# Performance work log

Measured on AMD Instinct MI355X. Metric: run time of the kernel, lower is better.

The kernel has to match this reference:

```python
import jax, jax.numpy as jnp
import numpy as np


def setup_inputs() -> dict:
    key = jax.random.key(0)
    k1, k2, k3, k4 = jax.random.split(key, 4)
    B, H, S, E, L = 2, 12, 256, 64, 25
    return {
        "attention_probs": jax.random.uniform(k1, (B, H, S, S), dtype=jnp.float32),
        "value_attentions": jax.random.normal(k2, (B, H, S, E), dtype=jnp.float32),
        "relative_positions": jax.random.normal(k3, (B, S, S, H * E), dtype=jnp.float32),
        "W": jax.random.normal(k4, (L, H * E), dtype=jnp.float32) * 0.02,
        "b": jnp.zeros((L,), dtype=jnp.float32),
    }


def reference(attention_probs, value_attentions, relative_positions, W, b):
    # Faithful translation of TransformerMHSLayer.forward:
    #   out[b,h,i,j,e] = p[b,h,i,j] * (v[b,h,j,e] + rel[b,i,j,h,e])
    #   pre[b,j,i,l]   = sum_{h,e} out[b,h,i,j,e] * W[l, h*E+e] + bias[l]
    #   logits[b,j,l,i] = pre[b,j,i,l]
    B, H, S, E = value_attentions.shape
    L = W.shape[0]
    Wr = W.reshape(L, H, E)                       # [L,H,E], matches h*E+e flattening
    rel = relative_positions.reshape(B, S, S, H, E)  # view(B,S,S,H,E)
    # value term: contract v with W per head, then weight by attention probs
    pre = jnp.einsum('bhij,bhje,lhe->bjil', attention_probs, value_attentions, Wr)
    # relative-position term (same attention weighting)
    pre = pre + jnp.einsum('bhij,bijhe,lhe->bjil', attention_probs, rel, Wr)
    pre = pre + b                                  # bias over label dim
    return pre.transpose(0, 1, 3, 2)               # [B, S(j), L, S(i)]
```

## Files before the change

### kernel.cpp

```cpp
#include <hip/hip_runtime.h>
#include <stdint.h>


#define Bb 2
#define Hh 12
#define Ss 256
#define Ee 64
#define Ll 25
#define Kk 768

typedef __attribute__((ext_vector_type(8))) short bf16x8;
typedef __attribute__((ext_vector_type(4))) float f32x4;

#define NFRAG (Hh * 4)
#define AB_BYTES ((size_t)NFRAG * 64 * 8 * 2)
#define PT_BYTES ((size_t)Bb * Ss * Hh * Ss * 4)
#define WV_BYTES ((size_t)Bb * Ss * Hh * 32 * 4)

__device__ __forceinline__ ushort f2bf(float x) {
    union { float f; uint32_t u; } u; u.f = x;
    uint32_t r = u.u + 0x7fff + ((u.u >> 16) & 1);
    return (ushort)(r >> 16);
}

__global__ void a_pack_kernel(const float* __restrict__ W, ushort* __restrict__ ab) {
    int idx = blockIdx.x * 256 + threadIdx.x;
    if (idx >= NFRAG * 64) return;
    int lane = idx & 63, fi = idx >> 6;
    int Lt = fi & 1, ks = (fi >> 1) & 1, h = fi >> 2;
    int l = Lt * 16 + (lane & 15);
    int k0 = h * Ee + ks * 32 + (lane >> 4) * 8;
    ushort* dst = ab + (size_t)idx * 8;
#pragma unroll
    for (int t = 0; t < 8; ++t)
        dst[t] = (l < Ll) ? f2bf(W[l * Kk + k0 + t]) : (ushort)0;
}

__global__ void p_transpose_kernel(const float* __restrict__ p,
                                   float* __restrict__ pt) {
    __shared__ float tile[32][33];
    const int bh = blockIdx.y;
    const int b = bh / Hh, h = bh % Hh;
    const int ti = blockIdx.x >> 3, tj = blockIdx.x & 7;
    const int tx = threadIdx.x & 31, ty = threadIdx.x >> 5;
#pragma unroll
    for (int s = 0; s < 4; ++s) {
        const int il = ty + 8 * s;
        tile[il][tx] = p[((size_t)(b * Hh + h) * Ss + ti * 32 + il) * Ss + tj * 32 + tx];
    }
    __syncthreads();
#pragma unroll
    for (int s = 0; s < 4; ++s) {
        const int jl = ty + 8 * s;
        pt[((size_t)(b * Ss + tj * 32 + jl) * Hh + h) * Ss + ti * 32 + tx] = tile[tx][jl];
    }
}

__global__ void wv_kernel(const float* __restrict__ W, const float* __restrict__ v,
                          float* __restrict__ wv) {
    const int bj = blockIdx.x;
    const int b = bj >> 8, j = bj & (Ss - 1);
    const int t = threadIdx.x;
    const int h = t >> 5, l = t & 31;
    float acc = 0.f;
    if (l < Ll) {
        const float* wrow = W + l * Kk + h * Ee;
        const float* vrow = v + ((size_t)(b * Hh + h) * Ss + j) * Ee;
#pragma unroll
        for (int e = 0; e < Ee; ++e) acc = __builtin_fmaf(wrow[e], vrow[e], acc);
    }
    wv[((size_t)bj * Hh + h) * 32 + l] = acc;
}

struct Buf {
    float4 r0, r1, r2, r3;
    bf16x8 A00, A01, A10, A11;
    float pv;
};

__global__ __launch_bounds__(256, 4) void mhs_pipe2(
    const float* __restrict__ pt,
    const float* __restrict__ rel,
    const ushort* __restrict__ ab,
    const float* __restrict__ wv,
    const float* __restrict__ bias,
    float* __restrict__ out)
{
    const int m = (blockIdx.x & 7) * 256 + (blockIdx.x >> 3);
    const int ig = m & 3, j = (m >> 2) & (Ss - 1), b = m >> 10;
    const int tid = threadIdx.x;
    const int w = tid >> 6, lane = tid & 63;
    const int col = lane & 15, grp = lane >> 4;
    const int iw = ig * 64 + w * 16 + col;

    const float* relp = rel + ((size_t)(b * Ss + iw) * Ss + j) * Kk + grp * 8;
    const ushort* abl = ab + lane * 8;
    const float* ptb = pt + ((size_t)(b * Ss + j) * Hh) * Ss + iw;
    const float* wvb = wv + ((size_t)(b * Ss + j) * Hh) * 32 + grp * 4;

    f32x4 acc0 = {0.f, 0.f, 0.f, 0.f};
    f32x4 acc1 = {0.f, 0.f, 0.f, 0.f};

    auto load = [&](Buf& o, int h) {
        const float* rb = relp + h * Ee;
        o.r0 = *(const float4*)(rb);
        o.r1 = *(const float4*)(rb + 4);
        o.r2 = *(const float4*)(rb + 32);
        o.r3 = *(const float4*)(rb + 36);
        const ushort* ap = abl + (size_t)h * 2048;
        o.A00 = *(const bf16x8*)(ap);
        o.A01 = *(const bf16x8*)(ap + 512);
        o.A10 = *(const bf16x8*)(ap + 1024);
        o.A11 = *(const bf16x8*)(ap + 1536);
        o.pv = ptb[h * Ss];
    };

    auto compute = [&](const Buf& o) {
        const float s = o.pv;
        bf16x8 B0, B1;
#pragma unroll
        for (int t = 0; t < 4; ++t) {
            B0[t]     = (short)f2bf(s * ((const float*)&o.r0)[t]);
            B0[t + 4] = (short)f2bf(s * ((const float*)&o.r1)[t]);
            B1[t]     = (short)f2bf(s * ((const float*)&o.r2)[t]);
            B1[t + 4] = (short)f2bf(s * ((const float*)&o.r3)[t]);
        }
        acc0 = __builtin_amdgcn_mfma_f32_16x16x32_bf16(o.A00, B0, acc0, 0, 0, 0);
        acc0 = __builtin_amdgcn_mfma_f32_16x16x32_bf16(o.A10, B1, acc0, 0, 0, 0);
        acc1 = __builtin_amdgcn_mfma_f32_16x16x32_bf16(o.A01, B0, acc1, 0, 0, 0);
        acc1 = __builtin_amdgcn_mfma_f32_16x16x32_bf16(o.A11, B1, acc1, 0, 0, 0);
    };

    Buf oa, ob;
    load(oa, 0);
#pragma unroll 1
    for (int h = 0; h < Hh; h += 2) {
        load(ob, h + 1);
        compute(oa);
        if (h + 2 < Hh) load(oa, h + 2);
        compute(ob);
    }

    f32x4 val0 = {0.f, 0.f, 0.f, 0.f};
    f32x4 val1 = {0.f, 0.f, 0.f, 0.f};
#pragma unroll
    for (int h = 0; h < Hh; ++h) {
        const float pvh = ptb[h * Ss];
        const f32x4 w0 = *(const f32x4*)(wvb + h * 32);
        const f32x4 w1 = *(const f32x4*)(wvb + h * 32 + 16);
        val0 += pvh * w0;
        val1 += pvh * w1;
    }
    acc0 += val0;
    acc1 += val1;

#pragma unroll
    for (int r = 0; r < 4; ++r) {
        const int l0 = grp * 4 + r;
        out[((size_t)(b * Ss + j) * Ll + l0) * Ss + iw] = acc0[r] + bias[l0];
        const int l1 = 16 + grp * 4 + r;
        if (l1 < Ll)
            out[((size_t)(b * Ss + j) * Ll + l1) * Ss + iw] = acc1[r] + bias[l1];
    }
}

__global__ __launch_bounds__(256, 4) void mhs_basic(
    const float* __restrict__ p, const float* __restrict__ v,
    const float* __restrict__ rel, const float* __restrict__ W,
    const float* __restrict__ bias, float* __restrict__ out)
{
    const int g = blockIdx.x;
    const int ig = g & 3, j = (g >> 2) & (Ss - 1), b = g >> 10;
    const int tid = threadIdx.x;
    const int w = tid >> 6, lane = tid & 63;
    const int col = lane & 15, grp = lane >> 4;
    const int iw = ig * 64 + w * 16 + col;
    const float* relp = rel + ((size_t)(b * Ss + iw) * Ss + j) * Kk + grp * 8;

    f32x4 acc0 = {0.f, 0.f, 0.f, 0.f}, acc1 = {0.f, 0.f, 0.f, 0.f};
#pragma unroll 1
    for (int h = 0; h < Hh; ++h) {
        bf16x8 A00, A01, A10, A11;
#pragma unroll
        for (int t = 0; t < 8; ++t) {
            const int kb = h * Ee + grp * 8 + t;
            const int la = col, lb = 16 + col;
            A00[t] = (short)f2bf(W[la * Kk + kb]);
            A01[t] = (lb < Ll) ? (short)f2bf(W[lb * Kk + kb]) : (short)0;
            A10[t] = (short)f2bf(W[la * Kk + kb + 32]);
            A11[t] = (lb < Ll) ? (short)f2bf(W[lb * Kk + kb + 32]) : (short)0;
        }
        const float* vbp = v + ((size_t)(b * Hh + h) * Ss + j) * Ee + grp * 8;
        const float4 va0 = *(const float4*)(vbp);
        const float4 va1 = *(const float4*)(vbp + 4);
        const float4 vc0 = *(const float4*)(vbp + 32);
        const float4 vc1 = *(const float4*)(vbp + 36);
        const float* rb = relp + h * Ee;
        const float4 c0 = *(const float4*)(rb);
        const float4 c1 = *(const float4*)(rb + 4);
        const float4 c2 = *(const float4*)(rb + 32);
        const float4 c3 = *(const float4*)(rb + 36);
        const float pv = p[((size_t)(b * Hh + h) * Ss + iw) * Ss + j];
        bf16x8 B0, B1;
#pragma unroll
        for (int t = 0; t < 4; ++t) {
            B0[t]     = (short)f2bf(((const float*)&c0)[t] + ((const float*)&va0)[t]);
            B0[t + 4] = (short)f2bf(((const float*)&c1)[t] + ((const float*)&va1)[t]);
            B1[t]     = (short)f2bf(((const float*)&c2)[t] + ((const float*)&vc0)[t]);
            B1[t + 4] = (short)f2bf(((const float*)&c3)[t] + ((const float*)&vc1)[t]);
        }
        f32x4 C0 = {0.f, 0.f, 0.f, 0.f}, C1 = {0.f, 0.f, 0.f, 0.f};
        C0 = __builtin_amdgcn_mfma_f32_16x16x32_bf16(A00, B0, C0, 0, 0, 0);
        C0 = __builtin_amdgcn_mfma_f32_16x16x32_bf16(A10, B1, C0, 0, 0, 0);
        C1 = __builtin_amdgcn_mfma_f32_16x16x32_bf16(A01, B0, C1, 0, 0, 0);
        C1 = __builtin_amdgcn_mfma_f32_16x16x32_bf16(A11, B1, C1, 0, 0, 0);
        acc0 += pv * C0;
        acc1 += pv * C1;
    }
#pragma unroll
    for (int r = 0; r < 4; ++r) {
        const int l0 = grp * 4 + r;
        out[((size_t)(b * Ss + j) * Ll + l0) * Ss + iw] = acc0[r] + bias[l0];
        const int l1 = 16 + grp * 4 + r;
        if (l1 < Ll)
            out[((size_t)(b * Ss + j) * Ll + l1) * Ss + iw] = acc1[r] + bias[l1];
    }
}

extern "C" void kernel_launch(void* const* d_in, const int* in_sizes, int n_in,
                              void* d_out, int out_size, void* d_ws, size_t ws_size,
                              hipStream_t stream) {
    const float* p    = (const float*)d_in[0];
    const float* v    = (const float*)d_in[1];
    const float* rel  = (const float*)d_in[2];
    const float* W    = (const float*)d_in[3];
    const float* bias = (const float*)d_in[4];
    float* out = (float*)d_out;

    const int nblk = Bb * Ss * 4;
    const bool full = ws_size >= AB_BYTES + PT_BYTES + WV_BYTES;

    if (full) {
        ushort* ab = (ushort*)d_ws;
        float* pt = (float*)((char*)d_ws + AB_BYTES);
        float* wvp = (float*)((char*)d_ws + AB_BYTES + PT_BYTES);
        hipLaunchKernelGGL(a_pack_kernel, dim3((NFRAG * 64 + 255) / 256), dim3(256),
                           0, stream, W, ab);
        hipLaunchKernelGGL(p_transpose_kernel, dim3(64, Bb * Hh), dim3(256),
                           0, stream, p, pt);
        hipLaunchKernelGGL(wv_kernel, dim3(Bb * Ss), dim3(Hh * 32),
                           0, stream, W, v, wvp);
        hipLaunchKernelGGL(mhs_pipe2, dim3(nblk), dim3(256), 0, stream,
                           pt, rel, ab, wvp, bias, out);
    } else {
        hipLaunchKernelGGL(mhs_basic, dim3(nblk), dim3(256), 0, stream,
                           p, v, rel, W, bias, out);
    }
}
```

Measured before the change: 123.6 us.

## Remap blocks to fixed query row i with j across lanes; drop p transpose

```diff
diff --git a/kernel.cpp b/kernel.cpp
--- a/kernel.cpp
+++ b/kernel.cpp
@@ -14,7 +14,6 @@
 
 #define NFRAG (Hh * 4)
 #define AB_BYTES ((size_t)NFRAG * 64 * 8 * 2)
-#define PT_BYTES ((size_t)Bb * Ss * Hh * Ss * 4)
 #define WV_BYTES ((size_t)Bb * Ss * Hh * 32 * 4)
 
 __device__ __forceinline__ ushort f2bf(float x) {
@@ -34,26 +33,6 @@
 #pragma unroll
     for (int t = 0; t < 8; ++t)
         dst[t] = (l < Ll) ? f2bf(W[l * Kk + k0 + t]) : (ushort)0;
-}
-
-__global__ void p_transpose_kernel(const float* __restrict__ p,
-                                   float* __restrict__ pt) {
-    __shared__ float tile[32][33];
-    const int bh = blockIdx.y;
-    const int b = bh / Hh, h = bh % Hh;
-    const int ti = blockIdx.x >> 3, tj = blockIdx.x & 7;
-    const int tx = threadIdx.x & 31, ty = threadIdx.x >> 5;
-#pragma unroll
-    for (int s = 0; s < 4; ++s) {
-        const int il = ty + 8 * s;
-        tile[il][tx] = p[((size_t)(b * Hh + h) * Ss + ti * 32 + il) * Ss + tj * 32 + tx];
-    }
-    __syncthreads();
-#pragma unroll
-    for (int s = 0; s < 4; ++s) {
-        const int jl = ty + 8 * s;
-        pt[((size_t)(b * Ss + tj * 32 + jl) * Hh + h) * Ss + ti * 32 + tx] = tile[tx][jl];
-    }
 }
 
 __global__ void wv_kernel(const float* __restrict__ W, const float* __restrict__ v,
@@ -78,24 +57,29 @@
     float pv;
 };
 
-__global__ __launch_bounds__(256, 4) void mhs_pipe2(
-    const float* __restrict__ pt,
+__global__ __launch_bounds__(256, 4) void mhs_jcol(
+    const float* __restrict__ p,
     const float* __restrict__ rel,
     const ushort* __restrict__ ab,
     const float* __restrict__ wv,
     const float* __restrict__ bias,
     float* __restrict__ out)
 {
-    const int m = (blockIdx.x & 7) * 256 + (blockIdx.x >> 3);
-    const int ig = m & 3, j = (m >> 2) & (Ss - 1), b = m >> 10;
+    const int bid = blockIdx.x;
+    const int xcd = bid & 7, idx = bid >> 3;
+    const int slot = idx >> 5, within = idx & 31;
+    const int g = slot * 8 + xcd;
+    const int n = g * 32 + within;
+    const int jb = n & 3, i = (n >> 2) & (Ss - 1), b = n >> 10;
+
     const int tid = threadIdx.x;
     const int w = tid >> 6, lane = tid & 63;
     const int col = lane & 15, grp = lane >> 4;
-    const int iw = ig * 64 + w * 16 + col;
-
-    const float* relp = rel + ((size_t)(b * Ss + iw) * Ss + j) * Kk + grp * 8;
+    const int j = jb * 64 + w * 16 + col;
+
+    const float* relp = rel + ((size_t)(b * Ss + i) * Ss + j) * Kk + grp * 8;
     const ushort* abl = ab + lane * 8;
-    const float* ptb = pt + ((size_t)(b * Ss + j) * Hh) * Ss + iw;
+    const float* pb = p + ((size_t)(b * Hh) * Ss + i) * Ss + j;
     const float* wvb = wv + ((size_t)(b * Ss + j) * Hh) * 32 + grp * 4;
 
     f32x4 acc0 = {0.f, 0.f, 0.f, 0.f};
@@ -112,7 +96,7 @@
         o.A01 = *(const bf16x8*)(ap + 512);
         o.A10 = *(const bf16x8*)(ap + 1024);
         o.A11 = *(const bf16x8*)(ap + 1536);
-        o.pv = ptb[h * Ss];
+        o.pv = pb[(size_t)h * Ss * Ss];
     };
 
     auto compute = [&](const Buf& o) {
@@ -145,7 +129,7 @@
     f32x4 val1 = {0.f, 0.f, 0.f, 0.f};
 #pragma unroll
     for (int h = 0; h < Hh; ++h) {
-        const float pvh = ptb[h * Ss];
+        const float pvh = pb[(size_t)h * Ss * Ss];
         const f32x4 w0 = *(const f32x4*)(wvb + h * 32);
         const f32x4 w1 = *(const f32x4*)(wvb + h * 32 + 16);
         val0 += pvh * w0;
@@ -157,25 +141,25 @@
 #pragma unroll
     for (int r = 0; r < 4; ++r) {
         const int l0 = grp * 4 + r;
-        out[((size_t)(b * Ss + j) * Ll + l0) * Ss + iw] = acc0[r] + bias[l0];
+        out[((size_t)(b * Ss + j) * Ll + l0) * Ss + i] = acc0[r] + bias[l0];
         const int l1 = 16 + grp * 4 + r;
         if (l1 < Ll)
-            out[((size_t)(b * Ss + j) * Ll + l1) * Ss + iw] = acc1[r] + bias[l1];
-    }
-}
-
-__global__ __launch_bounds__(256, 4) void mhs_basic(
+            out[((size_t)(b * Ss + j) * Ll + l1) * Ss + i] = acc1[r] + bias[l1];
+    }
+}
+
+__global__ __launch_bounds__(256, 4) void mhs_basic_j(
     const float* __restrict__ p, const float* __restrict__ v,
     const float* __restrict__ rel, const float* __restrict__ W,
     const float* __restrict__ bias, float* __restrict__ out)
 {
-    const int g = blockIdx.x;
-    const int ig = g & 3, j = (g >> 2) & (Ss - 1), b = g >> 10;
+    const int n = blockIdx.x;
+    const int jb = n & 3, i = (n >> 2) & (Ss - 1), b = n >> 10;
     const int tid = threadIdx.x;
     const int w = tid >> 6, lane = tid & 63;
     const int col = lane & 15, grp = lane >> 4;
-    const int iw = ig * 64 + w * 16 + col;
-    const float* relp = rel + ((size_t)(b * Ss + iw) * Ss + j) * Kk + grp * 8;
+    const int j = jb * 64 + w * 16 + col;
+    const float* relp = rel + ((size_t)(b * Ss + i) * Ss + j) * Kk + grp * 8;
 
     f32x4 acc0 = {0.f, 0.f, 0.f, 0.f}, acc1 = {0.f, 0.f, 0.f, 0.f};
 #pragma unroll 1
@@ -200,30 +184,27 @@
         const float4 c1 = *(const float4*)(rb + 4);
         const float4 c2 = *(const float4*)(rb + 32);
         const float4 c3 = *(const float4*)(rb + 36);
-        const float pv = p[((size_t)(b * Hh + h) * Ss + iw) * Ss + j];
+        const float pv = p[((size_t)(b * Hh + h) * Ss + i) * Ss + j];
         bf16x8 B0, B1;
 #pragma unroll
         for (int t = 0; t < 4; ++t) {
-            B0[t]     = (short)f2bf(((const float*)&c0)[t] + ((const float*)&va0)[t]);
-            B0[t + 4] = (short)f2bf(((const float*)&c1)[t] + ((const float*)&va1)[t]);
-            B1[t]     = (short)f2bf(((const float*)&c2)[t] + ((const float*)&vc0)[t]);
-            B1[t + 4] = (short)f2bf(((const float*)&c3)[t] + ((const float*)&vc1)[t]);
+            B0[t]     = (short)f2bf(pv * (((const float*)&c0)[t] + ((const float*)&va0)[t]));
+            B0[t + 4] = (short)f2bf(pv * (((const float*)&c1)[t] + ((const float*)&va1)[t]));
+            B1[t]     = (short)f2bf(pv * (((const float*)&c2)[t] + ((const float*)&vc0)[t]));
+            B1[t + 4] = (short)f2bf(pv * (((const float*)&c3)[t] + ((const float*)&vc1)[t]));
         }
-        f32x4 C0 = {0.f, 0.f, 0.f, 0.f}, C1 = {0.f, 0.f, 0.f, 0.f};
-        C0 = __builtin_amdgcn_mfma_f32_16x16x32_bf16(A00, B0, C0, 0, 0, 0);
-        C0 = __builtin_amdgcn_mfma_f32_16x16x32_bf16(A10, B1, C0, 0, 0, 0);
-        C1 = __builtin_amdgcn_mfma_f32_16x16x32_bf16(A01, B0, C1, 0, 0, 0);
-        C1 = __builtin_amdgcn_mfma_f32_16x16x32_bf16(A11, B1, C1, 0, 0, 0);
-        acc0 += pv * C0;
-        acc1 += pv * C1;
+        acc0 = __builtin_amdgcn_mfma_f32_16x16x32_bf16(A00, B0, acc0, 0, 0, 0);
+        acc0 = __builtin_amdgcn_mfma_f32_16x16x32_bf16(A10, B1, acc0, 0, 0, 0);
+        acc1 = __builtin_amdgcn_mfma_f32_16x16x32_bf16(A01, B0, acc1, 0, 0, 0);
+        acc1 = __builtin_amdgcn_mfma_f32_16x16x32_bf16(A11, B1, acc1, 0, 0, 0);
     }
 #pragma unroll
     for (int r = 0; r < 4; ++r) {
         const int l0 = grp * 4 + r;
-        out[((size_t)(b * Ss + j) * Ll + l0) * Ss + iw] = acc0[r] + bias[l0];
+        out[((size_t)(b * Ss + j) * Ll + l0) * Ss + i] = acc0[r] + bias[l0];
         const int l1 = 16 + grp * 4 + r;
         if (l1 < Ll)
-            out[((size_t)(b * Ss + j) * Ll + l1) * Ss + iw] = acc1[r] + bias[l1];
+            out[((size_t)(b * Ss + j) * Ll + l1) * Ss + i] = acc1[r] + bias[l1];
     }
 }
 
@@ -238,22 +219,19 @@
     float* out = (float*)d_out;
 
     const int nblk = Bb * Ss * 4;
-    const bool full = ws_size >= AB_BYTES + PT_BYTES + WV_BYTES;
+    const bool full = ws_size >= AB_BYTES + WV_BYTES;
 
     if (full) {
         ushort* ab = (ushort*)d_ws;
-        float* pt = (float*)((char*)d_ws + AB_BYTES);
-        float* wvp = (float*)((char*)d_ws + AB_BYTES + PT_BYTES);
+        float* wvp = (float*)((char*)d_ws + AB_BYTES);
         hipLaunchKernelGGL(a_pack_kernel, dim3((NFRAG * 64 + 255) / 256), dim3(256),
                            0, stream, W, ab);
-        hipLaunchKernelGGL(p_transpose_kernel, dim3(64, Bb * Hh), dim3(256),
-                           0, stream, p, pt);
         hipLaunchKernelGGL(wv_kernel, dim3(Bb * Ss), dim3(Hh * 32),
                            0, stream, W, v, wvp);
-        hipLaunchKernelGGL(mhs_pipe2, dim3(nblk), dim3(256), 0, stream,
-                           pt, rel, ab, wvp, bias, out);
+        hipLaunchKernelGGL(mhs_jcol, dim3(nblk), dim3(256), 0, stream,
+                           p, rel, ab, wvp, bias, out);
     } else {
-        hipLaunchKernelGGL(mhs_basic, dim3(nblk), dim3(256), 0, stream,
+        hipLaunchKernelGGL(mhs_basic_j, dim3(nblk), dim3(256), 0, stream,
                            p, v, rel, W, bias, out);
     }
 }
```

New measurement: 146.5 us. 1.19x slower.

## Stage rel rows through LDS with async global_load_lds and split heads across waves

Applied to the files above, without the earlier changes.

```diff
diff --git a/kernel.cpp b/kernel.cpp
--- a/kernel.cpp
+++ b/kernel.cpp
@@ -9,6 +9,14 @@
 #define Ll 25
 #define Kk 768
 
+#define JT 4
+#define NR 16
+#define CHF 256
+#define RSTR 268
+#define BUFF (NR * RSTR)
+#define REDF 2048
+#define NUNIT (JT * 3)
+
 typedef __attribute__((ext_vector_type(8))) short bf16x8;
 typedef __attribute__((ext_vector_type(4))) float f32x4;
 
@@ -16,6 +24,13 @@
 #define AB_BYTES ((size_t)NFRAG * 64 * 8 * 2)
 #define PT_BYTES ((size_t)Bb * Ss * Hh * Ss * 4)
 #define WV_BYTES ((size_t)Bb * Ss * Hh * 32 * 4)
+
+typedef const void __attribute__((address_space(1)))* gas_ptr;
+typedef void __attribute__((address_space(3)))* las_ptr;
+
+__device__ __forceinline__ void async_copy16(void* lds_dst, const void* g_src) {
+    __builtin_amdgcn_global_load_lds((gas_ptr)g_src, (las_ptr)lds_dst, 16, 0, 0);
+}
 
 __device__ __forceinline__ ushort f2bf(float x) {
     union { float f; uint32_t u; } u; u.f = x;
@@ -72,13 +87,7 @@
     wv[((size_t)bj * Hh + h) * 32 + l] = acc;
 }
 
-struct Buf {
-    float4 r0, r1, r2, r3;
-    bf16x8 A00, A01, A10, A11;
-    float pv;
-};
-
-__global__ __launch_bounds__(256, 4) void mhs_pipe2(
+__global__ __launch_bounds__(256, 3) void mhs_lds(
     const float* __restrict__ pt,
     const float* __restrict__ rel,
     const ushort* __restrict__ ab,
@@ -86,81 +95,100 @@
     const float* __restrict__ bias,
     float* __restrict__ out)
 {
-    const int m = (blockIdx.x & 7) * 256 + (blockIdx.x >> 3);
-    const int ig = m & 3, j = (m >> 2) & (Ss - 1), b = m >> 10;
+    __shared__ __align__(16) float lds[2 * BUFF + REDF];
+
+    const int n = blockIdx.x;
+    const int jt = n & 63, it = (n >> 6) & 15, b = n >> 10;
+    const int j0 = jt * JT, i0 = it * NR;
     const int tid = threadIdx.x;
     const int w = tid >> 6, lane = tid & 63;
     const int col = lane & 15, grp = lane >> 4;
-    const int iw = ig * 64 + w * 16 + col;
-
-    const float* relp = rel + ((size_t)(b * Ss + iw) * Ss + j) * Kk + grp * 8;
-    const ushort* abl = ab + lane * 8;
-    const float* ptb = pt + ((size_t)(b * Ss + j) * Hh) * Ss + iw;
-    const float* wvb = wv + ((size_t)(b * Ss + j) * Hh) * 32 + grp * 4;
+
+    auto stage = [&](int u, int d) {
+        const int jj = u / 3, c = u - jj * 3;
+#pragma unroll
+        for (int q = 0; q < 4; ++q) {
+            const int row = w * 4 + q;
+            const float* src = rel
+                + ((size_t)(b * Ss + i0 + row) * Ss + (j0 + jj)) * Kk
+                + c * CHF + lane * 4;
+            async_copy16(&lds[d * BUFF + row * RSTR], src);
+        }
+    };
 
     f32x4 acc0 = {0.f, 0.f, 0.f, 0.f};
     f32x4 acc1 = {0.f, 0.f, 0.f, 0.f};
 
-    auto load = [&](Buf& o, int h) {
-        const float* rb = relp + h * Ee;
-        o.r0 = *(const float4*)(rb);
-        o.r1 = *(const float4*)(rb + 4);
-        o.r2 = *(const float4*)(rb + 32);
-        o.r3 = *(const float4*)(rb + 36);
-        const ushort* ap = abl + (size_t)h * 2048;
-        o.A00 = *(const bf16x8*)(ap);
-        o.A01 = *(const bf16x8*)(ap + 512);
-        o.A10 = *(const bf16x8*)(ap + 1024);
-        o.A11 = *(const bf16x8*)(ap + 1536);
-        o.pv = ptb[h * Ss];
-    };
-
-    auto compute = [&](const Buf& o) {
-        const float s = o.pv;
+    stage(0, 0);
+    int buf = 0;
+#pragma unroll 1
+    for (int u = 0; u < NUNIT; ++u) {
+        __syncthreads();
+        if (u + 1 < NUNIT) stage(u + 1, buf ^ 1);
+
+        const int jj = u / 3, c = u - jj * 3;
+        const int j = j0 + jj;
+        const int h = c * 4 + w;
+
+        const ushort* ap = ab + (size_t)h * 2048 + lane * 8;
+        const bf16x8 A00 = *(const bf16x8*)(ap);
+        const bf16x8 A01 = *(const bf16x8*)(ap + 512);
+        const bf16x8 A10 = *(const bf16x8*)(ap + 1024);
+        const bf16x8 A11 = *(const bf16x8*)(ap + 1536);
+
+        const float pv = pt[((size_t)(b * Ss + j) * Hh + h) * Ss + i0 + col];
+
+        const float* rb = &lds[buf * BUFF + col * RSTR + w * 64 + grp * 8];
+        const float4 x0 = *(const float4*)(rb);
+        const float4 x1 = *(const float4*)(rb + 4);
+        const float4 y0 = *(const float4*)(rb + 32);
+        const float4 y1 = *(const float4*)(rb + 36);
+
         bf16x8 B0, B1;
 #pragma unroll
         for (int t = 0; t < 4; ++t) {
-            B0[t]     = (short)f2bf(s * ((const float*)&o.r0)[t]);
-            B0[t + 4] = (short)f2bf(s * ((const float*)&o.r1)[t]);
-            B1[t]     = (short)f2bf(s * ((const float*)&o.r2)[t]);
-            B1[t + 4] = (short)f2bf(s * ((const float*)&o.r3)[t]);
-        }
-        acc0 = __builtin_amdgcn_mfma_f32_16x16x32_bf16(o.A00, B0, acc0, 0, 0, 0);
-        acc0 = __builtin_amdgcn_mfma_f32_16x16x32_bf16(o.A10, B1, acc0, 0, 0, 0);
-        acc1 = __builtin_amdgcn_mfma_f32_16x16x32_bf16(o.A01, B0, acc1, 0, 0, 0);
-        acc1 = __builtin_amdgcn_mfma_f32_16x16x32_bf16(o.A11, B1, acc1, 0, 0, 0);
-    };
-
-    Buf oa, ob;
-    load(oa, 0);
-#pragma unroll 1
-    for (int h = 0; h < Hh; h += 2) {
-        load(ob, h + 1);
-        compute(oa);
-        if (h + 2 < Hh) load(oa, h + 2);
-        compute(ob);
-    }
-
-    f32x4 val0 = {0.f, 0.f, 0.f, 0.f};
-    f32x4 val1 = {0.f, 0.f, 0.f, 0.f};
-#pragma unroll
-    for (int h = 0; h < Hh; ++h) {
-        const float pvh = ptb[h * Ss];
-        const f32x4 w0 = *(const f32x4*)(wvb + h * 32);
-        const f32x4 w1 = *(const f32x4*)(wvb + h * 32 + 16);
-        val0 += pvh * w0;
-        val1 += pvh * w1;
-    }
-    acc0 += val0;
-    acc1 += val1;
-
-#pragma unroll
-    for (int r = 0; r < 4; ++r) {
-        const int l0 = grp * 4 + r;
-        out[((size_t)(b * Ss + j) * Ll + l0) * Ss + iw] = acc0[r] + bias[l0];
-        const int l1 = 16 + grp * 4 + r;
-        if (l1 < Ll)
-            out[((size_t)(b * Ss + j) * Ll + l1) * Ss + iw] = acc1[r] + bias[l1];
+            B0[t]     = (short)f2bf(pv * ((const float*)&x0)[t]);
+            B0[t + 4] = (short)f2bf(pv * ((const float*)&x1)[t]);
+            B1[t]     = (short)f2bf(pv * ((const float*)&y0)[t]);
+            B1[t + 4] = (short)f2bf(pv * ((const float*)&y1)[t]);
+        }
+        acc0 = __builtin_amdgcn_mfma_f32_16x16x32_bf16(A00, B0, acc0, 0, 0, 0);
+        acc0 = __builtin_amdgcn_mfma_f32_16x16x32_bf16(A10, B1, acc0, 0, 0, 0);
+        acc1 = __builtin_amdgcn_mfma_f32_16x16x32_bf16(A01, B0, acc1, 0, 0, 0);
+        acc1 = __builtin_amdgcn_mfma_f32_16x16x32_bf16(A11, B1, acc1, 0, 0, 0);
+
+        if (c == 2) {
+#pragma unroll
+            for (int hh = 0; hh < 3; ++hh) {
+                const int h2 = hh * 4 + w;
+                const float pvh = pt[((size_t)(b * Ss + j) * Hh + h2) * Ss + i0 + col];
+                const float* wp = wv + ((size_t)(b * Ss + j) * Hh + h2) * 32 + grp * 4;
+                const f32x4 w0 = *(const f32x4*)(wp);
+                const f32x4 w1 = *(const f32x4*)(wp + 16);
+                acc0 += pvh * w0;
+                acc1 += pvh * w1;
+            }
+            float* red = &lds[2 * BUFF];
+#pragma unroll
+            for (int r = 0; r < 4; ++r) {
+                red[w * 512 + (grp * 4 + r) * 16 + col]        = acc0[r];
+                red[w * 512 + (16 + grp * 4 + r) * 16 + col]   = acc1[r];
+            }
+            __syncthreads();
+#pragma unroll
+            for (int ss = 0; ss < 2; ++ss) {
+                const int s = tid + ss * 256;
+                const int lp = s >> 4, cc = s & 15;
+                if (lp < Ll) {
+                    const float val = red[s] + red[512 + s] + red[1024 + s]
+                                    + red[1536 + s] + bias[lp];
+                    out[((size_t)(b * Ss + j) * Ll + lp) * Ss + i0 + cc] = val;
+                }
+            }
+            acc0 = (f32x4){0.f, 0.f, 0.f, 0.f};
+            acc1 = (f32x4){0.f, 0.f, 0.f, 0.f};
+        }
+        buf ^= 1;
     }
 }
 
@@ -204,18 +232,15 @@
         bf16x8 B0, B1;
 #pragma unroll
         for (int t = 0; t < 4; ++t) {
-            B0[t]     = (short)f2bf(((const float*)&c0)[t] + ((const float*)&va0)[t]);
-            B0[t + 4] = (short)f2bf(((const float*)&c1)[t] + ((const float*)&va1)[t]);
-            B1[t]     = (short)f2bf(((const float*)&c2)[t] + ((const float*)&vc0)[t]);
-            B1[t + 4] = (short)f2bf(((const float*)&c3)[t] + ((const float*)&vc1)[t]);
-        }
-        f32x4 C0 = {0.f, 0.f, 0.f, 0.f}, C1 = {0.f, 0.f, 0.f, 0.f};
-        C0 = __builtin_amdgcn_mfma_f32_16x16x32_bf16(A00, B0, C0, 0, 0, 0);
-        C0 = __builtin_amdgcn_mfma_f32_16x16x32_bf16(A10, B1, C0, 0, 0, 0);
-        C1 = __builtin_amdgcn_mfma_f32_16x16x32_bf16(A01, B0, C1, 0, 0, 0);
-        C1 = __builtin_amdgcn_mfma_f32_16x16x32_bf16(A11, B1, C1, 0, 0, 0);
-        acc0 += pv * C0;
-        acc1 += pv * C1;
+            B0[t]     = (short)f2bf(pv * (((const float*)&c0)[t] + ((const float*)&va0)[t]));
+            B0[t + 4] = (short)f2bf(pv * (((const float*)&c1)[t] + ((const float*)&va1)[t]));
+            B1[t]     = (short)f2bf(pv * (((const float*)&c2)[t] + ((const float*)&vc0)[t]));
+            B1[t + 4] = (short)f2bf(pv * (((const float*)&c3)[t] + ((const float*)&vc1)[t]));
+        }
+        acc0 = __builtin_amdgcn_mfma_f32_16x16x32_bf16(A00, B0, acc0, 0, 0, 0);
+        acc0 = __builtin_amdgcn_mfma_f32_16x16x32_bf16(A10, B1, acc0, 0, 0, 0);
+        acc1 = __builtin_amdgcn_mfma_f32_16x16x32_bf16(A01, B0, acc1, 0, 0, 0);
+        acc1 = __builtin_amdgcn_mfma_f32_16x16x32_bf16(A11, B1, acc1, 0, 0, 0);
     }
 #pragma unroll
     for (int r = 0; r < 4; ++r) {
@@ -237,12 +262,11 @@
     const float* bias = (const float*)d_in[4];
     float* out = (float*)d_out;
 
-    const int nblk = Bb * Ss * 4;
     const bool full = ws_size >= AB_BYTES + PT_BYTES + WV_BYTES;
 
     if (full) {
         ushort* ab = (ushort*)d_ws;
-        float* pt = (float*)((char*)d_ws + AB_BYTES);
+        float* pt  = (float*)((char*)d_ws + AB_BYTES);
         float* wvp = (float*)((char*)d_ws + AB_BYTES + PT_BYTES);
         hipLaunchKernelGGL(a_pack_kernel, dim3((NFRAG * 64 + 255) / 256), dim3(256),
                            0, stream, W, ab);
@@ -250,10 +274,10 @@
                            0, stream, p, pt);
         hipLaunchKernelGGL(wv_kernel, dim3(Bb * Ss), dim3(Hh * 32),
                            0, stream, W, v, wvp);
-        hipLaunchKernelGGL(mhs_pipe2, dim3(nblk), dim3(256), 0, stream,
+        hipLaunchKernelGGL(mhs_lds, dim3(Bb * 16 * 64), dim3(256), 0, stream,
                            pt, rel, ab, wvp, bias, out);
     } else {
-        hipLaunchKernelGGL(mhs_basic, dim3(nblk), dim3(256), 0, stream,
+        hipLaunchKernelGGL(mhs_basic, dim3(Bb * Ss * 4), dim3(256), 0, stream,
                            p, v, rel, W, bias, out);
     }
 }
```

Result: no change. 125.1 us (+1.2%).
